# Optimization experiments

Hardware: AMD Instinct MI355X
Metric: run time of the kernel (lower is better)

The kernel has to match this reference:

```python
import jax, jax.numpy as jnp
import numpy as np

DIM = 384
HEADS = 12
HEAD_DIM = DIM // HEADS
SCALE = HEAD_DIM ** -0.5
HIDDEN = 4 * DIM
EPS = 1e-5


def _dwconv(x, w, b):
    # depthwise 3x3 conv, NCHW, kernel [C,1,3,3], groups=C
    y = jax.lax.conv_general_dilated(
        x, w, window_strides=(1, 1), padding='SAME',
        dimension_numbers=('NCHW', 'OIHW', 'NCHW'),
        feature_group_count=x.shape[1])
    return y + b[None, :, None, None]


def _layernorm(x, g, b):
    mu = jnp.mean(x, axis=-1, keepdims=True)
    var = jnp.mean(jnp.square(x - mu), axis=-1, keepdims=True)
    return (x - mu) * jax.lax.rsqrt(var + EPS) * g + b


def setup_inputs() -> dict:
    key = jax.random.key(0)
    ks = jax.random.split(key, 10)
    s = 0.02
    inp = {
        'x': jax.random.normal(ks[0], (32, DIM, 28, 28), dtype=jnp.float32),
        'cpe1_w': jax.random.normal(ks[1], (DIM, 1, 3, 3), dtype=jnp.float32) * s,
        'cpe1_b': jnp.zeros((DIM,), jnp.float32),
        'norm1_g': jnp.ones((DIM,), jnp.float32),
        'norm1_b': jnp.zeros((DIM,), jnp.float32),
        'qkv_w': jax.random.normal(ks[2], (3 * DIM, DIM), dtype=jnp.float32) * s,
        'proj_w': jax.random.normal(ks[3], (DIM, DIM), dtype=jnp.float32) * s,
        'proj_b': jnp.zeros((DIM,), jnp.float32),
        'cpe2_w': jax.random.normal(ks[4], (DIM, 1, 3, 3), dtype=jnp.float32) * s,
        'cpe2_b': jnp.zeros((DIM,), jnp.float32),
        'norm2_g': jnp.ones((DIM,), jnp.float32),
        'norm2_b': jnp.zeros((DIM,), jnp.float32),
        'fc1_w': jax.random.normal(ks[5], (HIDDEN, DIM), dtype=jnp.float32) * s,
        'fc1_b': jnp.zeros((HIDDEN,), jnp.float32),
        'fc2_w': jax.random.normal(ks[6], (DIM, HIDDEN), dtype=jnp.float32) * s,
        'fc2_b': jnp.zeros((DIM,), jnp.float32),
    }
    return inp


def reference(x, cpe1_w, cpe1_b, norm1_g, norm1_b, qkv_w, proj_w, proj_b,
              cpe2_w, cpe2_b, norm2_g, norm2_b, fc1_w, fc1_b, fc2_w, fc2_b):
    B, C, H, W = x.shape
    N = H * W
    # cpe1: depthwise conv residual (act = Identity)
    x = x + _dwconv(x, cpe1_w, cpe1_b)
    x = jnp.transpose(x.reshape(B, C, N), (0, 2, 1))  # [B, N, C]

    # channel attention
    cur = _layernorm(x, norm1_g, norm1_b)
    qkv = cur @ qkv_w.T  # [B, N, 3C]
    qkv = qkv.reshape(B, N, 3, HEADS, HEAD_DIM)
    q = qkv[:, :, 0]  # [B, N, h, d]
    k = qkv[:, :, 1] * SCALE
    v = qkv[:, :, 2]
    # attn = k^T @ v over tokens: [B, h, d, d]
    attn = jnp.einsum('bnhd,bnhe->bhde', k, v)
    attn = jax.nn.softmax(attn, axis=-1)
    # out[n,d] = sum_e attn[d,e] * q[n,e]
    out = jnp.einsum('bhde,bnhe->bnhd', attn, q).reshape(B, N, C)
    cur = out @ proj_w.T + proj_b
    x = x + cur

    # cpe2
    x = jnp.transpose(x, (0, 2, 1)).reshape(B, C, H, W)
    x = x + _dwconv(x, cpe2_w, cpe2_b)

    # MLP
    x = jnp.transpose(x.reshape(B, C, N), (0, 2, 1))  # [B, N, C]
    y = _layernorm(x, norm2_g, norm2_b)
    y = jax.nn.gelu(y @ fc1_w.T + fc1_b, approximate=False)
    y = y @ fc2_w.T + fc2_b
    x = x + y
    return jnp.transpose(x, (0, 2, 1)).reshape(B, C, H, W)
```

## Files before the change

kernel.cpp:

```cpp
#include <hip/hip_runtime.h>
#include <hip/hip_bf16.h>

#define CDIM 384
#define NHEADS 12
#define HDIM 32
#define HIDDEN 1536
#define BBATCH 32
#define HH 28
#define WW 28
#define NTOK 784
#define BN (BBATCH * NTOK)
#define LN_EPS 1e-5f
#define ATT_SCALE 0.17677669529663687f
#define YTILES 196
#define PERXCD 25

typedef __hip_bfloat16 bf16;
typedef __attribute__((ext_vector_type(8))) short bf16x8;
typedef __attribute__((ext_vector_type(4))) float f32x4;

__device__ __forceinline__ float ldf(const float* p) { return *p; }
__device__ __forceinline__ float ldf(const bf16* p) { return __bfloat162float(*p); }
__device__ __forceinline__ void stf(float* p, float v) { *p = v; }
__device__ __forceinline__ void stf(bf16* p, float v) { *p = __float2bfloat16(v); }

__device__ __forceinline__ short f2bs(float v) {
    bf16 t = __float2bfloat16(v);
    return *reinterpret_cast<short*>(&t);
}

__device__ __forceinline__ float gelu_f(float x) {
    float u = x * (0.7978845608f + 0.0356774081f * x * x);
    float e = __expf(-2.f * u);
    return x / (1.f + e);
}

__device__ __forceinline__ void gload16(const void* g, void* l) {
    __builtin_amdgcn_global_load_lds(
        (const __attribute__((address_space(1))) unsigned int*)g,
        (__attribute__((address_space(3))) unsigned int*)l, 16, 0, 0);
}

__global__ __launch_bounds__(256) void f2b4_k(
    const float* __restrict__ w0, const float* __restrict__ w1,
    const float* __restrict__ w2, const float* __restrict__ w3,
    bf16* __restrict__ dst)
{
    int i = blockIdx.x * 256 + threadIdx.x;
    const float* src; int off;
    if (i < 442368)       { src = w0; off = i; }
    else if (i < 589824)  { src = w1; off = i - 442368; }
    else if (i < 1179648) { src = w2; off = i - 589824; }
    else                  { src = w3; off = i - 1179648; }
    dst[i] = __float2bfloat16(src[off]);
}

__global__ __launch_bounds__(256) void wtr_k(const float* __restrict__ w,
                                             float* __restrict__ wt)
{
    int i = blockIdx.x * 256 + threadIdx.x;
    if (i < 9 * CDIM) {
        int k = i / CDIM, c = i % CDIM;
        wt[i] = w[c * 9 + k];
    }
}

__global__ __launch_bounds__(256) void dwconv_nchw_plane(
    const float* __restrict__ x, const float* __restrict__ w,
    const float* __restrict__ bias, float* __restrict__ y)
{
    __shared__ float sm[NTOK];
    int bc = blockIdx.x;
    int c = bc % CDIM;
    const float* xp = x + (size_t)bc * NTOK;
    int tid = threadIdx.x;
#pragma unroll
    for (int i = 0; i < 4; i++) {
        int p = tid + i * 256;
        if (p < NTOK) sm[p] = xp[p];
    }
    __syncthreads();
    const float* wp = w + c * 9;
    float w00 = wp[0], w01 = wp[1], w02 = wp[2];
    float w10 = wp[3], w11 = wp[4], w12 = wp[5];
    float w20 = wp[6], w21 = wp[7], w22 = wp[8];
    float bc_ = bias[c];
    float* yp = y + (size_t)bc * NTOK;
#pragma unroll
    for (int i = 0; i < 4; i++) {
        int p = tid + i * 256;
        if (p >= NTOK) break;
        int h = p / WW, wcol = p % WW;
        bool hm = h > 0, hp = h < HH - 1, wm = wcol > 0, wpv = wcol < WW - 1;
        float s = w11 * sm[p];
        if (hm)        s += w01 * sm[p - WW];
        if (hp)        s += w21 * sm[p + WW];
        if (wm)        s += w10 * sm[p - 1];
        if (wpv)       s += w12 * sm[p + 1];
        if (hm && wm)  s += w00 * sm[p - WW - 1];
        if (hm && wpv) s += w02 * sm[p - WW + 1];
        if (hp && wm)  s += w20 * sm[p + WW - 1];
        if (hp && wpv) s += w22 * sm[p + WW + 1];
        yp[p] = sm[p] + s + bc_;
    }
}

__global__ __launch_bounds__(256) void transpose_in(
    const float* __restrict__ in, float* __restrict__ out)
{
    __shared__ float t[32][33];
    int b = blockIdx.z;
    int n0 = blockIdx.y * 32;
    int c0 = blockIdx.x * 32;
    int tx = threadIdx.x, ty = threadIdx.y;
    for (int i = ty; i < 32; i += 8) {
        int n = n0 + tx;
        if (n < NTOK) t[i][tx] = in[((size_t)b * CDIM + c0 + i) * NTOK + n];
    }
    __syncthreads();
    for (int i = ty; i < 32; i += 8) {
        int n = n0 + i;
        if (n < NTOK) out[((size_t)b * NTOK + n) * CDIM + c0 + tx] = t[tx][i];
    }
}

__global__ __launch_bounds__(256) void dwconv_bnc_v2(
    const float* __restrict__ xin, const float* __restrict__ wt,
    const float* __restrict__ bias, float* __restrict__ xout)
{
    const int nblk = (BN * 96) / 256;
    const int per = nblk >> 3;
    int blk = blockIdx.x;
    int blk2 = (blk & 7) * per + (blk >> 3);
    int g4 = blk2 * 256 + threadIdx.x;
    int q = g4 % 96;
    int r = g4 / 96;
    int c = q * 4;
    int n = r % NTOK, b = r / NTOK;
    int h = n / WW, wcol = n % WW;
    const float4* base = (const float4*)(xin + (size_t)b * NTOK * CDIM);
    bool hm = h > 0, hp = h < HH - 1, wm = wcol > 0, wpv = wcol < WW - 1;

    float4 ctr = base[(size_t)n * 96 + q];
    float4 acc = {0.f, 0.f, 0.f, 0.f};

    const float4* w4 = (const float4*)wt;
#define TAP(k, cond, dn)                                            \
    if (cond) {                                                     \
        float4 vv = base[(size_t)(n + (dn)) * 96 + q];              \
        float4 ww = w4[(k) * 96 + q];                               \
        acc.x = fmaf(ww.x, vv.x, acc.x);                            \
        acc.y = fmaf(ww.y, vv.y, acc.y);                            \
        acc.z = fmaf(ww.z, vv.z, acc.z);                            \
        acc.w = fmaf(ww.w, vv.w, acc.w);                            \
    }
    TAP(0, hm && wm,   -WW - 1)
    TAP(1, hm,         -WW)
    TAP(2, hm && wpv,  -WW + 1)
    TAP(3, wm,         -1)
    { float4 ww = w4[4 * 96 + q];
      acc.x = fmaf(ww.x, ctr.x, acc.x); acc.y = fmaf(ww.y, ctr.y, acc.y);
      acc.z = fmaf(ww.z, ctr.z, acc.z); acc.w = fmaf(ww.w, ctr.w, acc.w); }
    TAP(5, wpv,        1)
    TAP(6, hp && wm,   WW - 1)
    TAP(7, hp,         WW)
    TAP(8, hp && wpv,  WW + 1)
#undef TAP
    float4 bb = *(const float4*)(bias + c);
    float4 outv;
    outv.x = ctr.x + acc.x + bb.x;
    outv.y = ctr.y + acc.y + bb.y;
    outv.z = ctr.z + acc.z + bb.z;
    outv.w = ctr.w + acc.w + bb.w;
    ((float4*)(xout))[g4] = outv;
}

template <typename TO>
__global__ __launch_bounds__(256) void layernorm_k(
    const float* __restrict__ in, const float* __restrict__ g,
    const float* __restrict__ b, TO* __restrict__ out)
{
    int wid = threadIdx.x >> 6;
    int lane = threadIdx.x & 63;
    size_t r = (size_t)blockIdx.x * 4 + wid;
    const float* row = in + r * CDIM;
    float v[6];
    float s = 0.f;
#pragma unroll
    for (int j = 0; j < 6; j++) { v[j] = row[lane + 64 * j]; s += v[j]; }
#pragma unroll
    for (int off = 32; off >= 1; off >>= 1) s += __shfl_xor(s, off);
    float mu = s * (1.f / CDIM);
    float q = 0.f;
#pragma unroll
    for (int j = 0; j < 6; j++) { float d = v[j] - mu; q += d * d; }
#pragma unroll
    for (int off = 32; off >= 1; off >>= 1) q += __shfl_xor(q, off);
    float rs = rsqrtf(q * (1.f / CDIM) + LN_EPS);
    TO* orow = out + r * CDIM;
#pragma unroll
    for (int j = 0; j < 6; j++) {
        int c = lane + 64 * j;
        stf(&orow[c], (v[j] - mu) * rs * g[c] + b[c]);
    }
}

template <int ACT, bool RES, typename TO>
__global__ __launch_bounds__(256, 4) void gemm_mfma(
    const short* __restrict__ Abf, const short* __restrict__ Bw,
    const float* __restrict__ bias, const float* __restrict__ res,
    TO* __restrict__ Co, int K, int M, int NX)
{
    int id = blockIdx.x;
    int xcd = id & 7, slot_ = id >> 3;
    int yloc = slot_ / NX, xx = slot_ - yloc * NX;
    int y = xcd * PERXCD + yloc;
    if (y >= YTILES) return;

    __shared__ __align__(16) short lds[16896];
    const int tid = threadIdx.x;
    const int wid = tid >> 6, lane = tid & 63;
    const int wrow = wid >> 1, wcol = wid & 1;
    const int quad = lane >> 4, lr = lane & 15;
    const int r0 = y * 128, m0 = xx * 128;

    const int srow = lane >> 2;
    const int sg   = (lane & 3) ^ (lane >> 4);
    const short* gA = Abf + (size_t)(r0 + wid * 32 + srow) * K + sg * 8;
    const short* gB = Bw  + (size_t)(m0 + wid * 32 + srow) * K + sg * 8;

    auto stage = [&](int k0, int p) {
        short* lA = lds + p * 8192 + wid * 1024;
        short* lB = lds + p * 8192 + 4096 + wid * 1024;
#pragma unroll
        for (int k = 0; k < 2; k++) {
            gload16(gA + k0 + (size_t)k * 16 * K, lA + k * 512);
            gload16(gB + k0 + (size_t)k * 16 * K, lB + k * 512);
        }
    };

    const int slot = (quad ^ (lr >> 2)) * 8;
    int fAoff[4], fBoff[4];
#pragma unroll
    for (int i = 0; i < 4; i++) {
        fAoff[i] = (wrow * 64 + i * 16 + lr) * 32 + slot;
        fBoff[i] = (wcol * 64 + i * 16 + lr) * 32 + slot;
    }

    f32x4 acc[4][4] = {};

    stage(0, 0);
    int p = 0;
    for (int k0 = 0; k0 < K; k0 += 32) {
        __syncthreads();
        if (k0 + 32 < K) stage(k0 + 32, p ^ 1);
        const short* As = lds + p * 8192;
        const short* Bs = As + 4096;
        bf16x8 av[4], bv[4];
#pragma unroll
        for (int i = 0; i < 4; i++) {
            av[i] = *(const bf16x8*)(As + fAoff[i]);
            bv[i] = *(const bf16x8*)(Bs + fBoff[i]);
        }
#pragma unroll
        for (int i = 0; i < 4; i++)
#pragma unroll
            for (int j = 0; j < 4; j++)
                acc[i][j] = __builtin_amdgcn_mfma_f32_16x16x32_bf16(
                    av[i], bv[j], acc[i][j], 0, 0, 0);
        p ^= 1;
    }

    if constexpr (sizeof(TO) == 4) {
#pragma unroll
        for (int i = 0; i < 4; i++) {
            int gr = r0 + wrow * 64 + i * 16 + quad * 4;
#pragma unroll
            for (int j = 0; j < 4; j++) {
                int gc = m0 + wcol * 64 + j * 16 + lr;
                float bb = bias ? bias[gc] : 0.f;
#pragma unroll
                for (int rr = 0; rr < 4; rr++) {
                    size_t idx = (size_t)(gr + rr) * M + gc;
                    float v = acc[i][j][rr] + bb;
                    if (RES) v += res[idx];
                    if (ACT == 1) v = gelu_f(v);
                    stf((float*)&Co[idx], v);
                }
            }
        }
    } else {
        __syncthreads();
        short* Cs = lds;
#pragma unroll
        for (int i = 0; i < 4; i++) {
            int lrow = wrow * 64 + i * 16 + quad * 4;
#pragma unroll
            for (int j = 0; j < 4; j++) {
                int lcol = wcol * 64 + j * 16 + lr;
                float bb = bias ? bias[m0 + lcol] : 0.f;
#pragma unroll
                for (int rr = 0; rr < 4; rr++) {
                    float v = acc[i][j][rr] + bb;
                    if (ACT == 1) v = gelu_f(v);
                    Cs[(lrow + rr) * 132 + lcol] = f2bs(v);
                }
            }
        }
        __syncthreads();
        short* co = (short*)Co;
#pragma unroll
        for (int s = 0; s < 16; s++) {
            int row = s * 8 + (tid >> 5);
            int seg = tid & 31;
            uint2 vv = *(const uint2*)(Cs + row * 132 + seg * 4);
            *(uint2*)(co + (size_t)(r0 + row) * M + m0 + seg * 4) = vv;
        }
    }
}

__global__ __launch_bounds__(256) void attn_k(
    const bf16* __restrict__ qkv, float* __restrict__ attn)
{
    int bh = blockIdx.x;
    int b = bh / NHEADS, h = bh % NHEADS;
    __shared__ float ks[64][32];
    __shared__ float vs[64][32];
    __shared__ float sm[32][33];
    int tid = threadIdx.x;
    int d = tid >> 3, e0 = (tid & 7) * 4;
    float acc[4] = {0.f, 0.f, 0.f, 0.f};
    for (int n0 = 0; n0 < NTOK; n0 += 64) {
#pragma unroll
        for (int i = 0; i < 8; i++) {
            int idx = tid + i * 256;
            int nn = idx >> 5, cc = idx & 31;
            int n = n0 + nn;
            float kv = 0.f, vv = 0.f;
            if (n < NTOK) {
                size_t base = ((size_t)b * NTOK + n) * (3 * CDIM);
                kv = ATT_SCALE * __bfloat162float(qkv[base + CDIM + h * HDIM + cc]);
                vv = __bfloat162float(qkv[base + 2 * CDIM + h * HDIM + cc]);
            }
            ks[nn][cc] = kv; vs[nn][cc] = vv;
        }
        __syncthreads();
#pragma unroll 8
        for (int nn = 0; nn < 64; nn++) {
            float kd = ks[nn][d];
#pragma unroll
            for (int j = 0; j < 4; j++) acc[j] += kd * vs[nn][e0 + j];
        }
        __syncthreads();
    }
#pragma unroll
    for (int j = 0; j < 4; j++) sm[d][e0 + j] = acc[j];
    __syncthreads();
    if (tid < 32) {
        float mx = -1e30f;
#pragma unroll
        for (int e = 0; e < 32; e++) mx = fmaxf(mx, sm[tid][e]);
        float ssum = 0.f;
        float ex[32];
#pragma unroll
        for (int e = 0; e < 32; e++) { ex[e] = expf(sm[tid][e] - mx); ssum += ex[e]; }
        float inv = 1.f / ssum;
        float* arow = attn + ((size_t)bh * 32 + tid) * 32;
#pragma unroll
        for (int e = 0; e < 32; e++) arow[e] = ex[e] * inv;
    }
}

__global__ __launch_bounds__(384) void apply_attn_k(
    const bf16* __restrict__ qkv, const float* __restrict__ attn,
    bf16* __restrict__ out)
{
    int b = blockIdx.x;
    int chunk = blockIdx.y;
    int tid = threadIdx.x;
    int h = tid >> 5;
    __shared__ float qs[8][CDIM];
    float at[32];
    const float4* ap = (const float4*)(attn + ((size_t)(b * NHEADS) * 32 + tid) * 32);
#pragma unroll
    for (int e4 = 0; e4 < 8; e4++) {
        float4 v = ap[e4];
        at[e4 * 4 + 0] = v.x; at[e4 * 4 + 1] = v.y;
        at[e4 * 4 + 2] = v.z; at[e4 * 4 + 3] = v.w;
    }
    int nbase = chunk * 56;
    for (int t0 = 0; t0 < 56; t0 += 8) {
        __syncthreads();
#pragma unroll
        for (int i = 0; i < 8; i++) {
            int n = nbase + t0 + i;
            qs[i][tid] = __bfloat162float(qkv[((size_t)b * NTOK + n) * (3 * CDIM) + tid]);
        }
        __syncthreads();
#pragma unroll
        for (int i = 0; i < 8; i++) {
            const float* qrow = &qs[i][h * 32];
            float s = 0.f;
#pragma unroll
            for (int e = 0; e < 32; e++) s += at[e] * qrow[e];
            int n = nbase + t0 + i;
            out[((size_t)b * NTOK + n) * CDIM + tid] = __float2bfloat16(s);
        }
    }
}

__global__ __launch_bounds__(256) void transpose_out(
    const float* __restrict__ in, float* __restrict__ out)
{
    __shared__ float t[32][33];
    int b = blockIdx.z;
    int n0 = blockIdx.y * 32;
    int c0 = blockIdx.x * 32;
    int tx = threadIdx.x, ty = threadIdx.y;
    for (int i = ty; i < 32; i += 8) {
        int n = n0 + i;
        if (n < NTOK) t[i][tx] = in[((size_t)b * NTOK + n) * CDIM + c0 + tx];
    }
    __syncthreads();
    for (int i = ty; i < 32; i += 8) {
        int c = c0 + i;
        int n = n0 + tx;
        if (n < NTOK) out[((size_t)b * CDIM + c) * NTOK + n] = t[tx][i];
    }
}

extern "C" void kernel_launch(void* const* d_in, const int* in_sizes, int n_in,
                              void* d_out, int out_size, void* d_ws, size_t ws_size,
                              hipStream_t stream) {
    const float* x      = (const float*)d_in[0];
    const float* cpe1_w = (const float*)d_in[1];
    const float* cpe1_b = (const float*)d_in[2];
    const float* n1g    = (const float*)d_in[3];
    const float* n1b    = (const float*)d_in[4];
    const float* qkv_w  = (const float*)d_in[5];
    const float* proj_w = (const float*)d_in[6];
    const float* proj_b = (const float*)d_in[7];
    const float* cpe2_w = (const float*)d_in[8];
    const float* cpe2_b = (const float*)d_in[9];
    const float* n2g    = (const float*)d_in[10];
    const float* n2b    = (const float*)d_in[11];
    const float* fc1_w  = (const float*)d_in[12];
    const float* fc1_b  = (const float*)d_in[13];
    const float* fc2_w  = (const float*)d_in[14];
    const float* fc2_b  = (const float*)d_in[15];

    const size_t A = (size_t)BN * CDIM;
    const size_t HA = A / 2;

    bf16* wqkv  = (bf16*)d_ws;
    bf16* wproj = wqkv + 442368;
    bf16* wfc1  = wproj + 147456;
    bf16* wfc2  = wfc1 + 589824;
    float* base = (float*)d_ws + 884736;

    float* xt        = base;
    bf16*  curb      = (bf16*)(base + A);
    bf16*  ylnb      = (bf16*)(base + A);
    bf16*  qkvb      = (bf16*)(base + A + HA);
    float* x3        = base + A + HA;
    bf16*  h1        = (bf16*)(base + A + HA + A);
    float* attnm     = base + 3 * A;
    bf16*  attn_outb = (bf16*)(base + 3 * A + 393216);
    float* finalb    = base;
    float* xconv     = base + (A * 7) / 2;
    float* cpe2_wt   = base + (A * 9) / 2;

    const int GEMM_GRID3  = 8 * PERXCD * 3;
    const int GEMM_GRID9  = 8 * PERXCD * 9;
    const int GEMM_GRID12 = 8 * PERXCD * 12;

    f2b4_k<<<1769472 / 256, 256, 0, stream>>>(qkv_w, proj_w, fc1_w, fc2_w, wqkv);
    wtr_k<<<14, 256, 0, stream>>>(cpe2_w, cpe2_wt);

    dwconv_nchw_plane<<<BBATCH * CDIM, 256, 0, stream>>>(x, cpe1_w, cpe1_b, xconv);
    transpose_in<<<dim3(CDIM / 32, (NTOK + 31) / 32, BBATCH), dim3(32, 8), 0, stream>>>(
        xconv, xt);
    layernorm_k<bf16><<<BN / 4, 256, 0, stream>>>(xt, n1g, n1b, curb);
    gemm_mfma<0, false, bf16><<<GEMM_GRID9, 256, 0, stream>>>(
        (const short*)curb, (const short*)wqkv, nullptr, nullptr, qkvb, 384, 1152, 9);
    attn_k<<<BBATCH * NHEADS, 256, 0, stream>>>(qkvb, attnm);
    apply_attn_k<<<dim3(BBATCH, 14), 384, 0, stream>>>(qkvb, attnm, attn_outb);
    gemm_mfma<0, true, float><<<GEMM_GRID3, 256, 0, stream>>>(
        (const short*)attn_outb, (const short*)wproj, proj_b, xt, xt, 384, 384, 3);
    dwconv_bnc_v2<<<(BN * 96) / 256, 256, 0, stream>>>(xt, cpe2_wt, cpe2_b, x3);
    layernorm_k<bf16><<<BN / 4, 256, 0, stream>>>(x3, n2g, n2b, ylnb);
    gemm_mfma<1, false, bf16><<<GEMM_GRID12, 256, 0, stream>>>(
        (const short*)ylnb, (const short*)wfc1, fc1_b, nullptr, h1, 384, 1536, 12);
    gemm_mfma<0, true, float><<<GEMM_GRID3, 256, 0, stream>>>(
        (const short*)h1, (const short*)wfc2, fc2_b, x3, finalb, 1536, 384, 3);
    transpose_out<<<dim3(CDIM / 32, (NTOK + 31) / 32, BBATCH), dim3(32, 8), 0, stream>>>(
        finalb, (float*)d_out);
}
```

Measured before the change: 451.2 us.

## Triple-buffer GEMM LDS staging with explicit vmcnt waits and new swizzle

The MFMA GEMM moves from a double-buffered LDS pipeline with a barrier at the top of each iteration to a three-stage ring buffer. The next-next tile is prefetched, and explicit s_waitcnt vmcnt counts let one group of loads stay in flight across the barrier. The LDS swizzle pattern for staging and fragment reads is also changed, likely to reduce bank conflicts. LDS use grows to 48KB per block, which may reduce occupancy relative to the 4-blocks-per-CU launch bound.

New measurement: 462.1 us. 1.02x slower.

```diff
diff --git a/kernel.cpp b/kernel.cpp
--- a/kernel.cpp
+++ b/kernel.cpp
@@ -217,7 +217,7 @@
     int y = xcd * PERXCD + yloc;
     if (y >= YTILES) return;
 
-    __shared__ __align__(16) short lds[16896];
+    __shared__ __align__(16) short lds[24576];
     const int tid = threadIdx.x;
     const int wid = tid >> 6, lane = tid & 63;
     const int wrow = wid >> 1, wcol = wid & 1;
@@ -225,7 +225,7 @@
     const int r0 = y * 128, m0 = xx * 128;
 
     const int srow = lane >> 2;
-    const int sg   = (lane & 3) ^ (lane >> 4);
+    const int sg   = (lane & 3) ^ ((lane >> 3) & 3);
     const short* gA = Abf + (size_t)(r0 + wid * 32 + srow) * K + sg * 8;
     const short* gB = Bw  + (size_t)(m0 + wid * 32 + srow) * K + sg * 8;
 
@@ -239,7 +239,7 @@
         }
     };
 
-    const int slot = (quad ^ (lr >> 2)) * 8;
+    const int slot = (quad ^ ((lr >> 1) & 3)) * 8;
     int fAoff[4], fBoff[4];
 #pragma unroll
     for (int i = 0; i < 4; i++) {
@@ -249,12 +249,20 @@
 
     f32x4 acc[4][4] = {};
 
+    const int nt = K >> 5;
     stage(0, 0);
-    int p = 0;
-    for (int k0 = 0; k0 < K; k0 += 32) {
-        __syncthreads();
-        if (k0 + 32 < K) stage(k0 + 32, p ^ 1);
-        const short* As = lds + p * 8192;
+    stage(32, 1);
+    asm volatile("s_waitcnt vmcnt(4)" ::: "memory");
+    __builtin_amdgcn_s_barrier();
+    __builtin_amdgcn_sched_barrier(0);
+
+    int cur = 0;
+    for (int t = 0; t < nt; ++t) {
+        if (t + 2 < nt) {
+            int pre = cur + 2; if (pre >= 3) pre -= 3;
+            stage((t + 2) << 5, pre);
+        }
+        const short* As = lds + cur * 8192;
         const short* Bs = As + 4096;
         bf16x8 av[4], bv[4];
 #pragma unroll
@@ -268,7 +276,15 @@
             for (int j = 0; j < 4; j++)
                 acc[i][j] = __builtin_amdgcn_mfma_f32_16x16x32_bf16(
                     av[i], bv[j], acc[i][j], 0, 0, 0);
-        p ^= 1;
+        if (t + 1 < nt) {
+            if (t + 2 < nt)
+                asm volatile("s_waitcnt vmcnt(4)" ::: "memory");
+            else
+                asm volatile("s_waitcnt vmcnt(0)" ::: "memory");
+            __builtin_amdgcn_s_barrier();
+            __builtin_amdgcn_sched_barrier(0);
+        }
+        cur = (cur == 2) ? 0 : cur + 1;
     }
 
     if constexpr (sizeof(TO) == 4) {
```

## Load GEMM B operand directly to registers and double K-tile depth to 64

Applied to the files above, without the earlier changes.

The GEMM now stages only the A tile through LDS, with a 64-wide K step and a new XOR swizzle. Each wave loads its B fragments straight from global memory into register double buffers. The main loop is unrolled over two LDS buffers so there is one barrier per 64-wide K step instead of per 32, and launch bounds drop to 3 blocks per SM to make room for the extra registers. The aim is to halve LDS traffic and cut barriers, at the cost of register pressure, lower occupancy, and less coalesced global reads of B.

Result: slower. 551.7 us (+22.3%).

```diff
diff --git a/kernel.cpp b/kernel.cpp
--- a/kernel.cpp
+++ b/kernel.cpp
@@ -206,7 +206,7 @@
 }
 
 template <int ACT, bool RES, typename TO>
-__global__ __launch_bounds__(256, 4) void gemm_mfma(
+__global__ __launch_bounds__(256, 3) void gemm_mfma(
     const short* __restrict__ Abf, const short* __restrict__ Bw,
     const float* __restrict__ bias, const float* __restrict__ res,
     TO* __restrict__ Co, int K, int M, int NX)
@@ -224,52 +224,70 @@
     const int quad = lane >> 4, lr = lane & 15;
     const int r0 = y * 128, m0 = xx * 128;
 
-    const int srow = lane >> 2;
-    const int sg   = (lane & 3) ^ (lane >> 4);
-    const short* gA = Abf + (size_t)(r0 + wid * 32 + srow) * K + sg * 8;
-    const short* gB = Bw  + (size_t)(m0 + wid * 32 + srow) * K + sg * 8;
+    const int sg = (lane & 7) ^ ((lane >> 3) & 7);
+    const short* gA = Abf + (size_t)(r0 + wid * 32 + (lane >> 3)) * K + sg * 8;
 
     auto stage = [&](int k0, int p) {
-        short* lA = lds + p * 8192 + wid * 1024;
-        short* lB = lds + p * 8192 + 4096 + wid * 1024;
-#pragma unroll
-        for (int k = 0; k < 2; k++) {
-            gload16(gA + k0 + (size_t)k * 16 * K, lA + k * 512);
-            gload16(gB + k0 + (size_t)k * 16 * K, lB + k * 512);
-        }
+        short* lA = lds + p * 8192 + wid * 2048;
+#pragma unroll
+        for (int k = 0; k < 4; k++)
+            gload16(gA + k0 + (size_t)k * 8 * K, lA + k * 512);
     };
 
-    const int slot = (quad ^ (lr >> 2)) * 8;
-    int fAoff[4], fBoff[4];
-#pragma unroll
-    for (int i = 0; i < 4; i++) {
-        fAoff[i] = (wrow * 64 + i * 16 + lr) * 32 + slot;
-        fBoff[i] = (wcol * 64 + i * 16 + lr) * 32 + slot;
-    }
+    const short* gB = Bw + (size_t)(m0 + wcol * 64 + lr) * K + quad * 8;
+    bf16x8 b0[8], b1[8];
+#define LOADB(bb, k0)                                                        \
+    {                                                                        \
+        _Pragma("unroll")                                                    \
+        for (int kh = 0; kh < 2; kh++)                                       \
+            _Pragma("unroll")                                                \
+            for (int j = 0; j < 4; j++)                                      \
+                bb[kh * 4 + j] = *(const bf16x8*)(gB + (size_t)j * 16 * K +  \
+                                                  (k0) + kh * 32);           \
+    }
+
+    int rowoff[4];
+#pragma unroll
+    for (int i = 0; i < 4; i++) rowoff[i] = (wrow * 64 + i * 16 + lr) * 64;
+    int slotk[2];
+#pragma unroll
+    for (int kh = 0; kh < 2; kh++) slotk[kh] = ((kh * 4 + quad) ^ (lr & 7)) * 8;
 
     f32x4 acc[4][4] = {};
 
+#define COMPUTE(As, bb)                                                      \
+    {                                                                        \
+        _Pragma("unroll")                                                    \
+        for (int kh = 0; kh < 2; kh++) {                                     \
+            bf16x8 av[4];                                                    \
+            _Pragma("unroll")                                                \
+            for (int i = 0; i < 4; i++)                                      \
+                av[i] = *(const bf16x8*)((As) + rowoff[i] + slotk[kh]);      \
+            _Pragma("unroll")                                                \
+            for (int i = 0; i < 4; i++)                                      \
+                _Pragma("unroll")                                            \
+                for (int j = 0; j < 4; j++)                                  \
+                    acc[i][j] = __builtin_amdgcn_mfma_f32_16x16x32_bf16(     \
+                        av[i], bb[kh * 4 + j], acc[i][j], 0, 0, 0);          \
+        }                                                                    \
+    }
+
+    const int nt = K >> 6;
     stage(0, 0);
-    int p = 0;
-    for (int k0 = 0; k0 < K; k0 += 32) {
+    LOADB(b0, 0);
+    __syncthreads();
+    for (int t = 0; t < nt; t += 2) {
+        if (t + 1 < nt) { stage((t + 1) << 6, 1); LOADB(b1, (t + 1) << 6); }
+        COMPUTE(lds, b0);
         __syncthreads();
-        if (k0 + 32 < K) stage(k0 + 32, p ^ 1);
-        const short* As = lds + p * 8192;
-        const short* Bs = As + 4096;
-        bf16x8 av[4], bv[4];
-#pragma unroll
-        for (int i = 0; i < 4; i++) {
-            av[i] = *(const bf16x8*)(As + fAoff[i]);
-            bv[i] = *(const bf16x8*)(Bs + fBoff[i]);
-        }
-#pragma unroll
-        for (int i = 0; i < 4; i++)
-#pragma unroll
-            for (int j = 0; j < 4; j++)
-                acc[i][j] = __builtin_amdgcn_mfma_f32_16x16x32_bf16(
-                    av[i], bv[j], acc[i][j], 0, 0, 0);
-        p ^= 1;
-    }
+        if (t + 1 < nt) {
+            if (t + 2 < nt) { stage((t + 2) << 6, 0); LOADB(b0, (t + 2) << 6); }
+            COMPUTE(lds + 8192, b1);
+            __syncthreads();
+        }
+    }
+#undef LOADB
+#undef COMPUTE
 
     if constexpr (sizeof(TO) == 4) {
 #pragma unroll
@@ -290,7 +308,6 @@
             }
         }
     } else {
-        __syncthreads();
         short* Cs = lds;
 #pragma unroll
         for (int i = 0; i < 4; i++) {
```

## Rewrite GEMM as 256x128 tile, 8-wave kernel with 4-stage LDS pipeline

Applied to the files above, without the earlier changes.

Replaces the 128x128, 4-wave, double-buffered MFMA GEMM with a 256x128 tile kernel that uses 8 waves. It adds a 4-slot LDS ring kept three stages ahead, with explicit vmcnt waits, sched barriers and setprio around the MFMA block. K becomes a template parameter so the loop count is known at compile time. The aim is to hide global-load latency better and raise the compute-to-load ratio. The cost is 96KB of LDS per block, which lowers occupancy, and fewer blocks per grid.

Result: slower. 486.4 us (+7.8%).

```diff
diff --git a/kernel.cpp b/kernel.cpp
--- a/kernel.cpp
+++ b/kernel.cpp
@@ -12,8 +12,8 @@
 #define BN (BBATCH * NTOK)
 #define LN_EPS 1e-5f
 #define ATT_SCALE 0.17677669529663687f
-#define YTILES 196
-#define PERXCD 25
+#define YT2 98
+#define PERXCD2 13
 
 typedef __hip_bfloat16 bf16;
 typedef __attribute__((ext_vector_type(8))) short bf16x8;
@@ -205,79 +205,90 @@
     }
 }
 
-template <int ACT, bool RES, typename TO>
-__global__ __launch_bounds__(256, 4) void gemm_mfma(
+template <int ACT, bool RES, typename TO, int K>
+__global__ __launch_bounds__(512, 2) void gemm_mfma8(
     const short* __restrict__ Abf, const short* __restrict__ Bw,
     const float* __restrict__ bias, const float* __restrict__ res,
-    TO* __restrict__ Co, int K, int M, int NX)
+    TO* __restrict__ Co, int M, int NX)
 {
     int id = blockIdx.x;
     int xcd = id & 7, slot_ = id >> 3;
     int yloc = slot_ / NX, xx = slot_ - yloc * NX;
-    int y = xcd * PERXCD + yloc;
-    if (y >= YTILES) return;
-
-    __shared__ __align__(16) short lds[16896];
+    int y = xcd * PERXCD2 + yloc;
+    if (y >= YT2) return;
+
+    __shared__ __align__(16) short lds[49152];
     const int tid = threadIdx.x;
     const int wid = tid >> 6, lane = tid & 63;
-    const int wrow = wid >> 1, wcol = wid & 1;
+    const int wr = wid >> 1, wc = wid & 1;
     const int quad = lane >> 4, lr = lane & 15;
-    const int r0 = y * 128, m0 = xx * 128;
-
-    const int srow = lane >> 2;
-    const int sg   = (lane & 3) ^ (lane >> 4);
-    const short* gA = Abf + (size_t)(r0 + wid * 32 + srow) * K + sg * 8;
-    const short* gB = Bw  + (size_t)(m0 + wid * 32 + srow) * K + sg * 8;
-
-    auto stage = [&](int k0, int p) {
-        short* lA = lds + p * 8192 + wid * 1024;
-        short* lB = lds + p * 8192 + 4096 + wid * 1024;
-#pragma unroll
-        for (int k = 0; k < 2; k++) {
-            gload16(gA + k0 + (size_t)k * 16 * K, lA + k * 512);
-            gload16(gB + k0 + (size_t)k * 16 * K, lB + k * 512);
-        }
+    const int r0 = y * 256, m0 = xx * 128;
+
+    const int sg = (lane & 3) ^ ((lane >> 3) & 3);
+    const short* gA = Abf + (size_t)(r0 + wid * 16 + (lane >> 2)) * K + sg * 8;
+    const short* gB = Bw  + (size_t)(m0 + wid * 16 + (lane >> 2)) * K + sg * 8;
+
+    auto stage = [&](int h) {
+        const int sl = h & 3;
+        short* lA = lds + sl * 12288 + wid * 512;
+        short* lB = lds + sl * 12288 + 8192 + wid * 512;
+        const size_t kof = (size_t)h * 32;
+        gload16(gA + kof, lA);
+        gload16(gA + kof + (size_t)128 * K, lA + 4096);
+        gload16(gB + kof, lB);
     };
 
-    const int slot = (quad ^ (lr >> 2)) * 8;
-    int fAoff[4], fBoff[4];
+    const int ksl = (quad ^ ((lr >> 1) & 3)) * 8;
+    int fA[4], fB[4];
 #pragma unroll
     for (int i = 0; i < 4; i++) {
-        fAoff[i] = (wrow * 64 + i * 16 + lr) * 32 + slot;
-        fBoff[i] = (wcol * 64 + i * 16 + lr) * 32 + slot;
+        fA[i] = (wr * 64 + i * 16 + lr) * 32 + ksl;
+        fB[i] = 8192 + (wc * 64 + i * 16 + lr) * 32 + ksl;
     }
 
     f32x4 acc[4][4] = {};
 
-    stage(0, 0);
-    int p = 0;
-    for (int k0 = 0; k0 < K; k0 += 32) {
-        __syncthreads();
-        if (k0 + 32 < K) stage(k0 + 32, p ^ 1);
-        const short* As = lds + p * 8192;
-        const short* Bs = As + 4096;
+    constexpr int NH = K / 32;
+    stage(0); stage(1); stage(2);
+    asm volatile("s_waitcnt vmcnt(6)" ::: "memory");
+    __builtin_amdgcn_s_barrier();
+    __builtin_amdgcn_sched_barrier(0);
+
+    for (int h = 0; h < NH; ++h) {
+        const short* S = lds + (h & 3) * 12288;
         bf16x8 av[4], bv[4];
 #pragma unroll
         for (int i = 0; i < 4; i++) {
-            av[i] = *(const bf16x8*)(As + fAoff[i]);
-            bv[i] = *(const bf16x8*)(Bs + fBoff[i]);
-        }
+            av[i] = *(const bf16x8*)(S + fA[i]);
+            bv[i] = *(const bf16x8*)(S + fB[i]);
+        }
+        __builtin_amdgcn_sched_barrier(0);
+        if (h + 3 < NH) stage(h + 3);
+        __builtin_amdgcn_sched_barrier(0);
+        if (h < NH - 3)       { asm volatile("s_waitcnt vmcnt(6)" ::: "memory"); }
+        else if (h == NH - 3) { asm volatile("s_waitcnt vmcnt(3)" ::: "memory"); }
+        else if (h == NH - 2) { asm volatile("s_waitcnt vmcnt(0)" ::: "memory"); }
+        __builtin_amdgcn_s_barrier();
+        __builtin_amdgcn_sched_barrier(0);
+        __builtin_amdgcn_s_setprio(1);
 #pragma unroll
         for (int i = 0; i < 4; i++)
 #pragma unroll
             for (int j = 0; j < 4; j++)
                 acc[i][j] = __builtin_amdgcn_mfma_f32_16x16x32_bf16(
                     av[i], bv[j], acc[i][j], 0, 0, 0);
-        p ^= 1;
+        __builtin_amdgcn_s_setprio(0);
+        __builtin_amdgcn_sched_barrier(0);
+        __builtin_amdgcn_s_barrier();
     }
 
     if constexpr (sizeof(TO) == 4) {
 #pragma unroll
         for (int i = 0; i < 4; i++) {
-            int gr = r0 + wrow * 64 + i * 16 + quad * 4;
+            int gr = r0 + wr * 64 + i * 16 + quad * 4;
 #pragma unroll
             for (int j = 0; j < 4; j++) {
-                int gc = m0 + wcol * 64 + j * 16 + lr;
+                int gc = m0 + wc * 64 + j * 16 + lr;
                 float bb = bias ? bias[gc] : 0.f;
 #pragma unroll
                 for (int rr = 0; rr < 4; rr++) {
@@ -290,14 +301,13 @@
             }
         }
     } else {
-        __syncthreads();
         short* Cs = lds;
 #pragma unroll
         for (int i = 0; i < 4; i++) {
-            int lrow = wrow * 64 + i * 16 + quad * 4;
+            int lrow = wr * 64 + i * 16 + quad * 4;
 #pragma unroll
             for (int j = 0; j < 4; j++) {
-                int lcol = wcol * 64 + j * 16 + lr;
+                int lcol = wc * 64 + j * 16 + lr;
                 float bb = bias ? bias[m0 + lcol] : 0.f;
 #pragma unroll
                 for (int rr = 0; rr < 4; rr++) {
@@ -311,7 +321,7 @@
         short* co = (short*)Co;
 #pragma unroll
         for (int s = 0; s < 16; s++) {
-            int row = s * 8 + (tid >> 5);
+            int row = s * 16 + (tid >> 5);
             int seg = tid & 31;
             uint2 vv = *(const uint2*)(Cs + row * 132 + seg * 4);
             *(uint2*)(co + (size_t)(r0 + row) * M + m0 + seg * 4) = vv;
@@ -470,9 +480,9 @@
     float* xconv     = base + (A * 7) / 2;
     float* cpe2_wt   = base + (A * 9) / 2;
 
-    const int GEMM_GRID3  = 8 * PERXCD * 3;
-    const int GEMM_GRID9  = 8 * PERXCD * 9;
-    const int GEMM_GRID12 = 8 * PERXCD * 12;
+    const int G8_3  = 8 * PERXCD2 * 3;
+    const int G8_9  = 8 * PERXCD2 * 9;
+    const int G8_12 = 8 * PERXCD2 * 12;
 
     f2b4_k<<<1769472 / 256, 256, 0, stream>>>(qkv_w, proj_w, fc1_w, fc2_w, wqkv);
     wtr_k<<<14, 256, 0, stream>>>(cpe2_w, cpe2_wt);
@@ -481,18 +491,18 @@
     transpose_in<<<dim3(CDIM / 32, (NTOK + 31) / 32, BBATCH), dim3(32, 8), 0, stream>>>(
         xconv, xt);
     layernorm_k<bf16><<<BN / 4, 256, 0, stream>>>(xt, n1g, n1b, curb);
-    gemm_mfma<0, false, bf16><<<GEMM_GRID9, 256, 0, stream>>>(
-        (const short*)curb, (const short*)wqkv, nullptr, nullptr, qkvb, 384, 1152, 9);
+    gemm_mfma8<0, false, bf16, 384><<<G8_9, 512, 0, stream>>>(
+        (const short*)curb, (const short*)wqkv, nullptr, nullptr, qkvb, 1152, 9);
     attn_k<<<BBATCH * NHEADS, 256, 0, stream>>>(qkvb, attnm);
     apply_attn_k<<<dim3(BBATCH, 14), 384, 0, stream>>>(qkvb, attnm, attn_outb);
-    gemm_mfma<0, true, float><<<GEMM_GRID3, 256, 0, stream>>>(
-        (const short*)attn_outb, (const short*)wproj, proj_b, xt, xt, 384, 384, 3);
+    gemm_mfma8<0, true, float, 384><<<G8_3, 512, 0, stream>>>(
+        (const short*)attn_outb, (const short*)wproj, proj_b, xt, xt, 384, 3);
     dwconv_bnc_v2<<<(BN * 96) / 256, 256, 0, stream>>>(xt, cpe2_wt, cpe2_b, x3);
     layernorm_k<bf16><<<BN / 4, 256, 0, stream>>>(x3, n2g, n2b, ylnb);
-    gemm_mfma<1, false, bf16><<<GEMM_GRID12, 256, 0, stream>>>(
-        (const short*)ylnb, (const short*)wfc1, fc1_b, nullptr, h1, 384, 1536, 12);
-    gemm_mfma<0, true, float><<<GEMM_GRID3, 256, 0, stream>>>(
-        (const short*)h1, (const short*)wfc2, fc2_b, x3, finalb, 1536, 384, 3);
+    gemm_mfma8<1, false, bf16, 384><<<G8_12, 512, 0, stream>>>(
+        (const short*)ylnb, (const short*)wfc1, fc1_b, nullptr, h1, 1536, 12);
+    gemm_mfma8<0, true, float, 1536><<<G8_3, 512, 0, stream>>>(
+        (const short*)h1, (const short*)wfc2, fc2_b, x3, finalb, 384, 3);
     transpose_out<<<dim3(CDIM / 32, (NTOK + 31) / 32, BBATCH), dim3(32, 8), 0, stream>>>(
         finalb, (float*)d_out);
 }
```
